# Kernel tuning notes

Hardware: AMD Instinct MI355X
Metric: run time of the kernel (lower is better)

The kernel has to match this reference:

```python
import jax, jax.numpy as jnp
import numpy as np
import math

B, T, D, H = 128, 512, 512, 512


def setup_inputs() -> dict:
    key = jax.random.key(0)
    ks = jax.random.split(key, 6)
    s = 1.0 / math.sqrt(H)
    return {
        "values": jax.random.normal(ks[0], (B, T, D), jnp.float32),
        "Deltas": jax.random.uniform(ks[1], (B, T, D), jnp.float32),
        "W_att": jax.random.normal(ks[2], (D, D), jnp.float32) * s,
        "b_att": jnp.zeros((D,), jnp.float32),
        "W_ih": jax.random.normal(ks[3], (4 * H, D), jnp.float32) * s,
        "W_hh": jax.random.normal(ks[4], (4 * H, H), jnp.float32) * s,
        "b_ih": jnp.zeros((4 * H,), jnp.float32),
        "b_hh": jnp.zeros((4 * H,), jnp.float32),
    }


def lstm_cell(x, h, c, W_ih, W_hh, b_ih, b_hh):
    # torch.nn.LSTMCell: gates ordered i, f, g, o
    g = x @ W_ih.T + b_ih + h @ W_hh.T + b_hh
    i, f, gg, o = jnp.split(g, 4, axis=-1)
    c2 = jax.nn.sigmoid(f) * c + jax.nn.sigmoid(i) * jnp.tanh(gg)
    h2 = jax.nn.sigmoid(o) * jnp.tanh(c2)
    return h2, c2


def reference(values, Deltas, W_att, b_att, W_ih, W_hh, b_ih, b_hh):
    Bn, Tn, Dn = values.shape
    Hn = W_hh.shape[1]
    # cumsum over time then reverse along time (reverse_tensor)
    Del = jnp.flip(jnp.cumsum(Deltas, axis=-2), axis=1)  # [B,T,D]
    v_att = values @ W_att.T + b_att                      # attn-projected inputs [B,T,D]
    # a_ij = bmm(atten_linear(values), values^T) -> [B,T,T]
    a_ij = jnp.einsum('btd,bsd->bts', v_att, values)
    h0 = jnp.zeros((Bn, Hn), values.dtype)
    c0 = jnp.zeros((Bn, Hn), values.dtype)

    def step(carry, x_t):
        h, c = carry
        h2, c2 = lstm_cell(x_t, h, c, W_ih, W_hh, b_ih, b_hh)
        return (h2, c2), (h2, c2)

    xs = jnp.swapaxes(v_att[:, :-1], 0, 1)  # [T-1, B, D]
    (h_last, _), (hs, cs) = jax.lax.scan(step, (h0, c0), xs)
    hs = jnp.swapaxes(hs, 0, 1)  # [B, T-1, H]
    cs = jnp.swapaxes(cs, 0, 1)  # [B, T-1, H]

    # attention-weighted cell-state mixing for the final step
    alpha = jax.nn.softmax(a_ij[:, -1, :-1], axis=-1)[..., None]  # [B,T-1,1]
    d = Del[:, 1:]                                                # [B,T-1,D]
    C_i = jnp.sum(alpha * cs / jnp.log(math.e + d), axis=1)       # [B,H]

    hT, cT = lstm_cell(v_att[:, -1], h_last, C_i, W_ih, W_hh, b_ih, b_hh)
    h_n = jnp.concatenate([hs, hT[:, None, :]], axis=1)  # [B,T,H]
    return h_n
```

## Files before the change

### kernel.cpp

```cpp
#include <hip/hip_runtime.h>
#include <cstdint>

#define DEVI __device__ __forceinline__

typedef unsigned short ushort_t;
typedef __attribute__((ext_vector_type(8))) short s16x8;
typedef __attribute__((ext_vector_type(4))) float f32x4;

DEVI ushort_t f2bf(float f) {
  uint32_t u = __builtin_bit_cast(uint32_t, f);
  u += 0x7fffu + ((u >> 16) & 1u);
  return (ushort_t)(u >> 16);
}
DEVI float bf2f(ushort_t u) {
  uint32_t x = ((uint32_t)u) << 16;
  return __builtin_bit_cast(float, x);
}
DEVI float sigmoidf_(float x) { return 1.0f / (1.0f + __expf(-x)); }
DEVI float tanhf_(float x) {
  float e = __expf(-2.0f * fabsf(x));
  float r = (1.0f - e) / (1.0f + e);
  return copysignf(r, x);
}

DEVI void issue_load_h16(s16x8& dst, const ushort_t* p) {
  asm volatile("global_load_dwordx4 %0, %1, off sc0 sc1" : "=v"(dst) : "v"(p));
}
DEVI int load_flag(const int* p) {
  int r;
  asm volatile("global_load_dword %0, %1, off sc0 sc1\n\ts_waitcnt vmcnt(0)"
               : "=v"(r) : "v"(p) : "memory");
  return r;
}
DEVI void store_h(ushort_t* p, uint32_t v) {
  asm volatile("global_store_short %0, %1, off sc0 sc1" :: "v"(p), "v"(v) : "memory");
}
DEVI void store_flag(int* p, int v) {
  asm volatile("global_store_dword %0, %1, off sc0 sc1" :: "v"(p), "v"(v) : "memory");
}
DEVI void wait_vm0() { asm volatile("s_waitcnt vmcnt(0)" ::: "memory"); }

__global__ void cast_kernel(const float* __restrict__ in, ushort_t* __restrict__ out, long n) {
  long i = ((long)blockIdx.x * blockDim.x + threadIdx.x) * 8;
  if (i >= n) return;
  float4 a = *(const float4*)(in + i);
  float4 b = *(const float4*)(in + i + 4);
  union { s16x8 v; ushort_t u[8]; } r;
  r.u[0] = f2bf(a.x); r.u[1] = f2bf(a.y); r.u[2] = f2bf(a.z); r.u[3] = f2bf(a.w);
  r.u[4] = f2bf(b.x); r.u[5] = f2bf(b.y); r.u[6] = f2bf(b.z); r.u[7] = f2bf(b.w);
  *(s16x8*)(out + i) = r.v;
}

__global__ void transpose512(const float* __restrict__ in, float* __restrict__ out) {
  __shared__ float tile[32][33];
  int bx = blockIdx.x * 32, by = blockIdx.y * 32;
  int tx = threadIdx.x, ty = threadIdx.y;
  for (int i = 0; i < 32; i += 8)
    tile[ty + i][tx] = in[(by + ty + i) * 512 + bx + tx];
  __syncthreads();
  for (int i = 0; i < 32; i += 8)
    out[(bx + ty + i) * 512 + by + tx] = tile[tx][ty + i];
}

__global__ __launch_bounds__(256, 2)
void gemm_bt(const ushort_t* __restrict__ A, const ushort_t* __restrict__ B,
             const float* __restrict__ bias0, const float* __restrict__ bias1,
             ushort_t* __restrict__ C, int N, int K) {
  __shared__ __align__(16) ushort_t As[128 * 64];
  __shared__ __align__(16) ushort_t Bs[128 * 64];
  const int tid = threadIdx.x;
  const int lane = tid & 63, wv = tid >> 6;
  const int wm = wv >> 1, wn = wv & 1;
  const int l15 = lane & 15, l4 = lane >> 4;
  const long m0 = (long)blockIdx.x * 128;
  const int n0 = blockIdx.y * 128;
  const int nkt = K / 64;

  f32x4 acc[4][4] = {};

  int soff[4];
#pragma unroll
  for (int i = 0; i < 4; ++i) {
    int c = tid + i * 256;
    int r = c >> 3, ks = c & 7;
    soff[i] = r * 64 + ((ks ^ (r & 7)) << 3);
  }

#pragma unroll
  for (int i = 0; i < 4; ++i) {
    int c = tid + i * 256; int r = c >> 3; int ks = c & 7;
    *(s16x8*)&As[soff[i]] = *(const s16x8*)&A[(m0 + r) * K + ks * 8];
    *(s16x8*)&Bs[soff[i]] = *(const s16x8*)&B[(long)(n0 + r) * K + ks * 8];
  }
  __syncthreads();

  for (int kt = 0; kt < nkt; ++kt) {
    s16x8 ra[4], rb[4];
    const bool more = (kt + 1 < nkt);
    if (more) {
      const long kb = (long)(kt + 1) * 64;
#pragma unroll
      for (int i = 0; i < 4; ++i) {
        int c = tid + i * 256; int r = c >> 3; int ks = c & 7;
        ra[i] = *(const s16x8*)&A[(m0 + r) * K + kb + ks * 8];
        rb[i] = *(const s16x8*)&B[(long)(n0 + r) * K + kb + ks * 8];
      }
    }
#pragma unroll
    for (int kk = 0; kk < 2; ++kk) {
      s16x8 af[4], bfv[4];
      int slot = kk * 4 + l4;
#pragma unroll
      for (int i = 0; i < 4; ++i) {
        int rA = wm * 64 + i * 16 + l15;
        af[i] = *(const s16x8*)&As[rA * 64 + ((slot ^ (rA & 7)) << 3)];
        int rB = wn * 64 + i * 16 + l15;
        bfv[i] = *(const s16x8*)&Bs[rB * 64 + ((slot ^ (rB & 7)) << 3)];
      }
#pragma unroll
      for (int i = 0; i < 4; ++i)
#pragma unroll
        for (int j = 0; j < 4; ++j)
          acc[i][j] = __builtin_amdgcn_mfma_f32_16x16x32_bf16(af[i], bfv[j], acc[i][j], 0, 0, 0);
    }
    __syncthreads();
    if (more) {
#pragma unroll
      for (int i = 0; i < 4; ++i) {
        *(s16x8*)&As[soff[i]] = ra[i];
        *(s16x8*)&Bs[soff[i]] = rb[i];
      }
      __syncthreads();
    }
  }
#pragma unroll
  for (int i = 0; i < 4; ++i) {
#pragma unroll
    for (int j = 0; j < 4; ++j) {
#pragma unroll
      for (int r = 0; r < 4; ++r) {
        long m = m0 + wm * 64 + i * 16 + l4 * 4 + r;
        int n = n0 + wn * 64 + j * 16 + l15;
        float v = acc[i][j][r] + bias0[n];
        if (bias1) v += bias1[n];
        C[m * (long)N + n] = f2bf(v);
      }
    }
  }
}

__global__ void vT_kernel(const float* __restrict__ values, const float* __restrict__ W_attT,
                          const float* __restrict__ b_att, float* __restrict__ vT) {
  int b = blockIdx.y;
  int n = blockIdx.x * 256 + threadIdx.x;
  __shared__ float xr[512];
  const float* row = values + ((long)b * 512 + 511) * 512;
  for (int k = threadIdx.x; k < 512; k += 256) xr[k] = row[k];
  __syncthreads();
  float acc = b_att[n];
  for (int k = 0; k < 512; ++k) acc += xr[k] * W_attT[k * 512 + n];
  vT[b * 512 + n] = acc;
}

__global__ void dtot_kernel(const float* __restrict__ Deltas, float* __restrict__ Dtot) {
  int idx = blockIdx.x * 256 + threadIdx.x;
  int b = idx >> 9, ch = idx & 511;
  const float* p = Deltas + (long)b * 512 * 512 + ch;
  float s = 0.0f;
  for (int t = 0; t < 511; ++t) s += p[(long)t * 512];
  Dtot[idx] = s;
}

__global__ void logits_kernel(const float* __restrict__ values, const float* __restrict__ vT,
                              float* __restrict__ logits) {
  int b = blockIdx.y;
  int wave = threadIdx.x >> 6, lane = threadIdx.x & 63;
  float vreg[8];
  const float* vtb = vT + b * 512;
#pragma unroll
  for (int j = 0; j < 8; ++j) vreg[j] = vtb[lane * 8 + j];
  int s0 = blockIdx.x * 64 + wave * 16;
  for (int si = 0; si < 16; ++si) {
    int s = s0 + si;
    if (s >= 511) break;
    const float* row = values + ((long)b * 512 + s) * 512 + lane * 8;
    float4 a = *(const float4*)row;
    float4 c = *(const float4*)(row + 4);
    float d = a.x * vreg[0] + a.y * vreg[1] + a.z * vreg[2] + a.w * vreg[3] +
              c.x * vreg[4] + c.y * vreg[5] + c.z * vreg[6] + c.w * vreg[7];
#pragma unroll
    for (int off = 32; off; off >>= 1) d += __shfl_xor(d, off);
    if (lane == 0) logits[b * 512 + s] = d;
  }
}

__global__ void softmax_kernel(float* __restrict__ logits) {
  int b = blockIdx.x, tid = threadIdx.x;
  __shared__ float wmax[4], wsum[4];
  float v0 = (tid < 511) ? logits[b * 512 + tid] : -1e30f;
  float v1 = (tid + 256 < 511) ? logits[b * 512 + tid + 256] : -1e30f;
  float m = fmaxf(v0, v1);
#pragma unroll
  for (int off = 32; off; off >>= 1) m = fmaxf(m, __shfl_xor(m, off));
  if ((tid & 63) == 0) wmax[tid >> 6] = m;
  __syncthreads();
  m = fmaxf(fmaxf(wmax[0], wmax[1]), fmaxf(wmax[2], wmax[3]));
  float e0 = (tid < 511) ? __expf(v0 - m) : 0.0f;
  float e1 = (tid + 256 < 511) ? __expf(v1 - m) : 0.0f;
  float s = e0 + e1;
#pragma unroll
  for (int off = 32; off; off >>= 1) s += __shfl_xor(s, off);
  if ((tid & 63) == 0) wsum[tid >> 6] = s;
  __syncthreads();
  s = wsum[0] + wsum[1] + wsum[2] + wsum[3];
  float inv = 1.0f / s;
  __syncthreads();
  if (tid < 511) logits[b * 512 + tid] = e0 * inv;
  if (tid + 256 < 511) logits[b * 512 + tid + 256] = e1 * inv;
}

__global__ __launch_bounds__(256, 1)
void scan_kernel(const float* __restrict__ W_hh, const ushort_t* __restrict__ Gx,
                 const float* __restrict__ alpha, const float* __restrict__ Dtot,
                 const float* __restrict__ Deltas, ushort_t* __restrict__ hbuf,
                 int* __restrict__ flags, float* __restrict__ out) {
  __shared__ __align__(16) ushort_t whh[64 * 512];
  __shared__ float gbuf[4][16][17];
  const int tid = threadIdx.x;
  const int bg = blockIdx.x & 7, hc = blockIdx.x >> 3;
  const int b0 = bg * 16, n0 = hc * 16;
  const int lane = tid & 63, wv = tid >> 6;
  const int l15 = lane & 15, l4 = lane >> 4;
  const int eb = tid >> 4, eh = tid & 15;
  const int bglob = b0 + eb, hglob = n0 + eh;

  for (int idx = tid; idx < 64 * 512; idx += 256) {
    int r = idx >> 9, k = idx & 511;
    int grow = (r >> 4) * 512 + n0 + (r & 15);
    float v = W_hh[(long)grow * 512 + k];
    int off = r * 512 + ((((k >> 3) ^ (r & 7)) << 3) | (k & 7));
    whh[off] = f2bf(v);
  }
  float c_state = 0.0f, Cacc = 0.0f;
  float running = Dtot[bglob * 512 + hglob];
  __syncthreads();

  const int brow = wv * 16 + l15;
  s16x8 bfr[16];
#pragma unroll
  for (int kk = 0; kk < 16; ++kk) {
    int slot = (kk * 4 + l4) ^ (brow & 7);
    bfr[kk] = *(const s16x8*)&whh[brow * 512 + (slot << 3)];
  }
  const long gxcol = wv * 512 + n0 + l15;

  for (int t = 0; t < 512; ++t) {
    float a_t = 0.0f, delta_t = 0.0f;
    if (t < 511) {
      a_t = alpha[bglob * 512 + t];
      delta_t = Deltas[((long)bglob * 512 + (510 - t)) * 512 + hglob];
    }
    float gx[4];
#pragma unroll
    for (int r = 0; r < 4; ++r)
      gx[r] = bf2f(Gx[((long)(b0 + l4 * 4 + r) * 512 + t) * 2048 + gxcol]);

    if (t > 0) {
      if (wv == 0) {
        const int* fp = flags + ((long)bg * 512 + (t - 1)) * 32 + (lane & 31);
        int g = 0;
        while (!__all(load_flag(fp) != 0)) {
          __builtin_amdgcn_s_sleep(1);
          if (++g > (1 << 20)) break;
        }
      }
      __syncthreads();
    }

    const ushort_t* hb = hbuf + ((t & 1) * 8 + bg) * (16 * 512);
    s16x8 afr[16];
#pragma unroll
    for (int kk = 0; kk < 16; ++kk)
      issue_load_h16(afr[kk], hb + l15 * 512 + kk * 32 + l4 * 8);
    wait_vm0();
    __builtin_amdgcn_sched_barrier(0);

    f32x4 acc = {0.0f, 0.0f, 0.0f, 0.0f};
#pragma unroll
    for (int kk = 0; kk < 16; ++kk)
      acc = __builtin_amdgcn_mfma_f32_16x16x32_bf16(afr[kk], bfr[kk], acc, 0, 0, 0);
#pragma unroll
    for (int r = 0; r < 4; ++r)
      gbuf[wv][l4 * 4 + r][l15] = acc[r] + gx[r];
    __syncthreads();

    float gi = gbuf[0][eb][eh], gf = gbuf[1][eb][eh];
    float gg = gbuf[2][eb][eh], go = gbuf[3][eb][eh];
    float cin = (t == 511) ? Cacc : c_state;
    float cnew = sigmoidf_(gf) * cin + sigmoidf_(gi) * tanhf_(gg);
    float hnew = sigmoidf_(go) * tanhf_(cnew);
    out[((long)bglob * 512 + t) * 512 + hglob] = hnew;
    if (t < 511) {
      c_state = cnew;
      float rl = 1.0f / __logf(2.71828182845904523f + running);
      Cacc += a_t * cnew * rl;
      running -= delta_t;
      ushort_t* hw = hbuf + (((t + 1) & 1) * 8 + bg) * (16 * 512);
      store_h(hw + eb * 512 + hglob, (uint32_t)f2bf(hnew));
      wait_vm0();
      __syncthreads();
      if (tid == 0)
        store_flag(flags + ((long)bg * 512 + t) * 32 + hc, 1);
    }
  }
}

extern "C" void kernel_launch(void* const* d_in, const int* in_sizes, int n_in,
                              void* d_out, int out_size, void* d_ws, size_t ws_size,
                              hipStream_t stream) {
  const float* values = (const float*)d_in[0];
  const float* Deltas = (const float*)d_in[1];
  const float* W_att  = (const float*)d_in[2];
  const float* b_att  = (const float*)d_in[3];
  const float* W_ih   = (const float*)d_in[4];
  const float* W_hh   = (const float*)d_in[5];
  const float* b_ih   = (const float*)d_in[6];
  const float* b_hh   = (const float*)d_in[7];
  float* out = (float*)d_out;

  char* ws = (char*)d_ws;
  size_t off = 0;
  auto alloc = [&](size_t bytes) -> void* {
    void* p = ws + off;
    off += (bytes + 255) & ~(size_t)255;
    return p;
  };
  ushort_t* values_bf = (ushort_t*)alloc(67108864ull);
  ushort_t* v_att_bf  = (ushort_t*)alloc(67108864ull);
  ushort_t* Gx        = (ushort_t*)alloc(268435456ull);
  ushort_t* W_att_bf  = (ushort_t*)alloc(524288ull);
  ushort_t* W_ih_bf   = (ushort_t*)alloc(2097152ull);
  float*    W_attT    = (float*)alloc(1048576ull);
  float*    vT        = (float*)alloc(262144ull);
  float*    Dtot      = (float*)alloc(262144ull);
  float*    alpha     = (float*)alloc(262144ull);
  ushort_t* hbuf      = (ushort_t*)alloc(262144ull);
  int*      flags     = (int*)alloc(524288ull);

  hipMemsetAsync(hbuf, 0, 262144ull + 524288ull, stream);

  cast_kernel<<<33554432 / 8 / 256, 256, 0, stream>>>(values, values_bf, 33554432L);
  cast_kernel<<<262144 / 8 / 256, 256, 0, stream>>>(W_att, W_att_bf, 262144L);
  cast_kernel<<<1048576 / 8 / 256, 256, 0, stream>>>(W_ih, W_ih_bf, 1048576L);
  transpose512<<<dim3(16, 16), dim3(32, 8), 0, stream>>>(W_att, W_attT);

  gemm_bt<<<dim3(512, 4), 256, 0, stream>>>(values_bf, W_att_bf, b_att, nullptr,
                                            v_att_bf, 512, 512);
  gemm_bt<<<dim3(512, 16), 256, 0, stream>>>(v_att_bf, W_ih_bf, b_ih, b_hh,
                                             Gx, 2048, 512);

  vT_kernel<<<dim3(2, 128), 256, 0, stream>>>(values, W_attT, b_att, vT);
  dtot_kernel<<<256, 256, 0, stream>>>(Deltas, Dtot);
  logits_kernel<<<dim3(8, 128), 256, 0, stream>>>(values, vT, alpha);
  softmax_kernel<<<128, 256, 0, stream>>>(alpha);

  scan_kernel<<<256, 256, 0, stream>>>(W_hh, Gx, alpha, Dtot, Deltas, hbuf, flags, out);
}
```

Before: 2.528 ms.

## Fold W_att into W_ih and replace flag barrier with tagged h values

Precomputes the combined weight W_ih·W_att and its bias, so the input-gate GEMM reads values directly and the separate v_att projection GEMM is removed. The scan kernel drops the per-step flag array and block barrier: each h element is stored as a 32-bit word holding the step tag and the bf16 value, and readers spin until every tag matches. The MFMA work is reorganised so each wave covers a K-slice for all four gates, with the partial sums reduced through double-buffered shared memory. This cuts GEMM traffic and per-step synchronisation latency, at the cost of doubling the h buffer size and rounding the fused weight to bf16.

```diff
diff --git a/kernel.cpp b/kernel.cpp
--- a/kernel.cpp
+++ b/kernel.cpp
@@ -5,6 +5,7 @@
 
 typedef unsigned short ushort_t;
 typedef __attribute__((ext_vector_type(8))) short s16x8;
+typedef __attribute__((ext_vector_type(4))) int i32x4;
 typedef __attribute__((ext_vector_type(4))) float f32x4;
 
 DEVI ushort_t f2bf(float f) {
@@ -23,19 +24,10 @@
   return copysignf(r, x);
 }
 
-DEVI void issue_load_h16(s16x8& dst, const ushort_t* p) {
+DEVI void load_tag16(i32x4& dst, const uint32_t* p) {
   asm volatile("global_load_dwordx4 %0, %1, off sc0 sc1" : "=v"(dst) : "v"(p));
 }
-DEVI int load_flag(const int* p) {
-  int r;
-  asm volatile("global_load_dword %0, %1, off sc0 sc1\n\ts_waitcnt vmcnt(0)"
-               : "=v"(r) : "v"(p) : "memory");
-  return r;
-}
-DEVI void store_h(ushort_t* p, uint32_t v) {
-  asm volatile("global_store_short %0, %1, off sc0 sc1" :: "v"(p), "v"(v) : "memory");
-}
-DEVI void store_flag(int* p, int v) {
+DEVI void store_tagged(uint32_t* p, uint32_t v) {
   asm volatile("global_store_dword %0, %1, off sc0 sc1" :: "v"(p), "v"(v) : "memory");
 }
 DEVI void wait_vm0() { asm volatile("s_waitcnt vmcnt(0)" ::: "memory"); }
@@ -141,12 +133,26 @@
       for (int r = 0; r < 4; ++r) {
         long m = m0 + wm * 64 + i * 16 + l4 * 4 + r;
         int n = n0 + wn * 64 + j * 16 + l15;
-        float v = acc[i][j][r] + bias0[n];
+        float v = acc[i][j][r];
+        if (bias0) v += bias0[n];
         if (bias1) v += bias1[n];
         C[m * (long)N + n] = f2bf(v);
       }
     }
   }
+}
+
+__global__ void bias_combo_kernel(const float* __restrict__ W_ih, const float* __restrict__ b_att,
+                                  const float* __restrict__ b_ih, const float* __restrict__ b_hh,
+                                  float* __restrict__ bc) {
+  int n = blockIdx.x * 256 + threadIdx.x;
+  __shared__ float ba[512];
+  for (int k = threadIdx.x; k < 512; k += 256) ba[k] = b_att[k];
+  __syncthreads();
+  float s = b_ih[n] + b_hh[n];
+  const float* row = W_ih + (long)n * 512;
+  for (int k = 0; k < 512; ++k) s += row[k] * ba[k];
+  bc[n] = s;
 }
 
 __global__ void vT_kernel(const float* __restrict__ values, const float* __restrict__ W_attT,
@@ -222,10 +228,10 @@
 __global__ __launch_bounds__(256, 1)
 void scan_kernel(const float* __restrict__ W_hh, const ushort_t* __restrict__ Gx,
                  const float* __restrict__ alpha, const float* __restrict__ Dtot,
-                 const float* __restrict__ Deltas, ushort_t* __restrict__ hbuf,
-                 int* __restrict__ flags, float* __restrict__ out) {
+                 const float* __restrict__ Deltas, uint32_t* __restrict__ hbuf32,
+                 float* __restrict__ out) {
   __shared__ __align__(16) ushort_t whh[64 * 512];
-  __shared__ float gbuf[4][16][17];
+  __shared__ float gbuf[2][4][4][16][16];
   const int tid = threadIdx.x;
   const int bg = blockIdx.x & 7, hc = blockIdx.x >> 3;
   const int b0 = bg * 16, n0 = hc * 16;
@@ -245,14 +251,17 @@
   float running = Dtot[bglob * 512 + hglob];
   __syncthreads();
 
-  const int brow = wv * 16 + l15;
-  s16x8 bfr[16];
-#pragma unroll
-  for (int kk = 0; kk < 16; ++kk) {
-    int slot = (kk * 4 + l4) ^ (brow & 7);
-    bfr[kk] = *(const s16x8*)&whh[brow * 512 + (slot << 3)];
-  }
-  const long gxcol = wv * 512 + n0 + l15;
+  s16x8 bfr[4][4];
+#pragma unroll
+  for (int g = 0; g < 4; ++g) {
+    const int brow = g * 16 + l15;
+#pragma unroll
+    for (int kk4 = 0; kk4 < 4; ++kk4) {
+      int ks = wv * 128 + kk4 * 32 + l4 * 8;
+      int slot = (ks >> 3) ^ (brow & 7);
+      bfr[g][kk4] = *(const s16x8*)&whh[brow * 512 + (slot << 3)];
+    }
+  }
 
   for (int t = 0; t < 512; ++t) {
     float a_t = 0.0f, delta_t = 0.0f;
@@ -260,57 +269,76 @@
       a_t = alpha[bglob * 512 + t];
       delta_t = Deltas[((long)bglob * 512 + (510 - t)) * 512 + hglob];
     }
-    float gx[4];
-#pragma unroll
-    for (int r = 0; r < 4; ++r)
-      gx[r] = bf2f(Gx[((long)(b0 + l4 * 4 + r) * 512 + t) * 2048 + gxcol]);
-
-    if (t > 0) {
-      if (wv == 0) {
-        const int* fp = flags + ((long)bg * 512 + (t - 1)) * 32 + (lane & 31);
-        int g = 0;
-        while (!__all(load_flag(fp) != 0)) {
-          __builtin_amdgcn_s_sleep(1);
-          if (++g > (1 << 20)) break;
-        }
-      }
-      __syncthreads();
-    }
-
-    const ushort_t* hb = hbuf + ((t & 1) * 8 + bg) * (16 * 512);
-    s16x8 afr[16];
-#pragma unroll
-    for (int kk = 0; kk < 16; ++kk)
-      issue_load_h16(afr[kk], hb + l15 * 512 + kk * 32 + l4 * 8);
-    wait_vm0();
-    __builtin_amdgcn_sched_barrier(0);
-
-    f32x4 acc = {0.0f, 0.0f, 0.0f, 0.0f};
-#pragma unroll
-    for (int kk = 0; kk < 16; ++kk)
-      acc = __builtin_amdgcn_mfma_f32_16x16x32_bf16(afr[kk], bfr[kk], acc, 0, 0, 0);
-#pragma unroll
-    for (int r = 0; r < 4; ++r)
-      gbuf[wv][l4 * 4 + r][l15] = acc[r] + gx[r];
+    float gxv[4];
+#pragma unroll
+    for (int g = 0; g < 4; ++g)
+      gxv[g] = bf2f(Gx[((long)bglob * 512 + t) * 2048 + g * 512 + hglob]);
+
+    const uint32_t* hb = hbuf32 + ((t & 1) * 8 + bg) * 8192 + l15 * 512 + wv * 128 + l4 * 8;
+    const uint32_t expect = (uint32_t)t << 16;
+    i32x4 q[8];
+    int guard = 0;
+    for (;;) {
+#pragma unroll
+      for (int kk4 = 0; kk4 < 4; ++kk4) {
+        load_tag16(q[kk4 * 2], hb + kk4 * 32);
+        load_tag16(q[kk4 * 2 + 1], hb + kk4 * 32 + 4);
+      }
+      wait_vm0();
+      __builtin_amdgcn_sched_barrier(0);
+      uint32_t bad = 0;
+#pragma unroll
+      for (int i = 0; i < 8; ++i) {
+        bad |= (uint32_t)q[i][0] ^ expect;
+        bad |= (uint32_t)q[i][1] ^ expect;
+        bad |= (uint32_t)q[i][2] ^ expect;
+        bad |= (uint32_t)q[i][3] ^ expect;
+      }
+      if (!__any((bad & 0xffff0000u) != 0)) break;
+      __builtin_amdgcn_s_sleep(1);
+      if (++guard > (1 << 16)) break;
+    }
+    s16x8 afr[4];
+#pragma unroll
+    for (int kk4 = 0; kk4 < 4; ++kk4) {
+#pragma unroll
+      for (int j = 0; j < 4; ++j) {
+        afr[kk4][j]     = (short)((uint32_t)q[kk4 * 2][j] & 0xffffu);
+        afr[kk4][j + 4] = (short)((uint32_t)q[kk4 * 2 + 1][j] & 0xffffu);
+      }
+    }
+    f32x4 acc[4] = {};
+#pragma unroll
+    for (int kk4 = 0; kk4 < 4; ++kk4)
+#pragma unroll
+      for (int g = 0; g < 4; ++g)
+        acc[g] = __builtin_amdgcn_mfma_f32_16x16x32_bf16(afr[kk4], bfr[g][kk4], acc[g], 0, 0, 0);
+
+    const int p = t & 1;
+#pragma unroll
+    for (int g = 0; g < 4; ++g)
+#pragma unroll
+      for (int r = 0; r < 4; ++r)
+        gbuf[p][wv][g][l4 * 4 + r][l15] = acc[g][r];
     __syncthreads();
 
-    float gi = gbuf[0][eb][eh], gf = gbuf[1][eb][eh];
-    float gg = gbuf[2][eb][eh], go = gbuf[3][eb][eh];
+    float gate[4];
+#pragma unroll
+    for (int g = 0; g < 4; ++g)
+      gate[g] = gbuf[p][0][g][eb][eh] + gbuf[p][1][g][eb][eh] +
+                gbuf[p][2][g][eb][eh] + gbuf[p][3][g][eb][eh] + gxv[g];
+
     float cin = (t == 511) ? Cacc : c_state;
-    float cnew = sigmoidf_(gf) * cin + sigmoidf_(gi) * tanhf_(gg);
-    float hnew = sigmoidf_(go) * tanhf_(cnew);
+    float cnew = sigmoidf_(gate[1]) * cin + sigmoidf_(gate[0]) * tanhf_(gate[2]);
+    float hnew = sigmoidf_(gate[3]) * tanhf_(cnew);
     out[((long)bglob * 512 + t) * 512 + hglob] = hnew;
     if (t < 511) {
       c_state = cnew;
       float rl = 1.0f / __logf(2.71828182845904523f + running);
       Cacc += a_t * cnew * rl;
       running -= delta_t;
-      ushort_t* hw = hbuf + (((t + 1) & 1) * 8 + bg) * (16 * 512);
-      store_h(hw + eb * 512 + hglob, (uint32_t)f2bf(hnew));
-      wait_vm0();
-      __syncthreads();
-      if (tid == 0)
-        store_flag(flags + ((long)bg * 512 + t) * 32 + hc, 1);
+      uint32_t w = ((uint32_t)(t + 1) << 16) | (uint32_t)f2bf(hnew);
+      store_tagged(hbuf32 + (((t + 1) & 1) * 8 + bg) * 8192 + eb * 512 + hglob, w);
     }
   }
 }
@@ -336,27 +364,29 @@
     return p;
   };
   ushort_t* values_bf = (ushort_t*)alloc(67108864ull);
-  ushort_t* v_att_bf  = (ushort_t*)alloc(67108864ull);
   ushort_t* Gx        = (ushort_t*)alloc(268435456ull);
-  ushort_t* W_att_bf  = (ushort_t*)alloc(524288ull);
   ushort_t* W_ih_bf   = (ushort_t*)alloc(2097152ull);
+  ushort_t* Wc_bf     = (ushort_t*)alloc(2097152ull);
   float*    W_attT    = (float*)alloc(1048576ull);
+  ushort_t* W_attT_bf = (ushort_t*)alloc(524288ull);
   float*    vT        = (float*)alloc(262144ull);
   float*    Dtot      = (float*)alloc(262144ull);
   float*    alpha     = (float*)alloc(262144ull);
-  ushort_t* hbuf      = (ushort_t*)alloc(262144ull);
-  int*      flags     = (int*)alloc(524288ull);
-
-  hipMemsetAsync(hbuf, 0, 262144ull + 524288ull, stream);
+  float*    bias_c    = (float*)alloc(8192ull);
+  uint32_t* hbuf32    = (uint32_t*)alloc(524288ull);
+
+  hipMemsetAsync(hbuf32, 0, 524288ull, stream);
 
   cast_kernel<<<33554432 / 8 / 256, 256, 0, stream>>>(values, values_bf, 33554432L);
-  cast_kernel<<<262144 / 8 / 256, 256, 0, stream>>>(W_att, W_att_bf, 262144L);
   cast_kernel<<<1048576 / 8 / 256, 256, 0, stream>>>(W_ih, W_ih_bf, 1048576L);
   transpose512<<<dim3(16, 16), dim3(32, 8), 0, stream>>>(W_att, W_attT);
-
-  gemm_bt<<<dim3(512, 4), 256, 0, stream>>>(values_bf, W_att_bf, b_att, nullptr,
-                                            v_att_bf, 512, 512);
-  gemm_bt<<<dim3(512, 16), 256, 0, stream>>>(v_att_bf, W_ih_bf, b_ih, b_hh,
+  cast_kernel<<<262144 / 8 / 256, 256, 0, stream>>>(W_attT, W_attT_bf, 262144L);
+
+  gemm_bt<<<dim3(16, 4), 256, 0, stream>>>(W_ih_bf, W_attT_bf, nullptr, nullptr,
+                                           Wc_bf, 512, 512);
+  bias_combo_kernel<<<8, 256, 0, stream>>>(W_ih, b_att, b_ih, b_hh, bias_c);
+
+  gemm_bt<<<dim3(512, 16), 256, 0, stream>>>(values_bf, Wc_bf, bias_c, nullptr,
                                              Gx, 2048, 512);
 
   vT_kernel<<<dim3(2, 128), 256, 0, stream>>>(values, W_attT, b_att, vT);
@@ -364,5 +394,5 @@
   logits_kernel<<<dim3(8, 128), 256, 0, stream>>>(values, vT, alpha);
   softmax_kernel<<<128, 256, 0, stream>>>(alpha);
 
-  scan_kernel<<<256, 256, 0, stream>>>(W_hh, Gx, alpha, Dtot, Deltas, hbuf, flags, out);
-}
+  scan_kernel<<<256, 256, 0, stream>>>(W_hh, Gx, alpha, Dtot, Deltas, hbuf32, out);
+}
```

Result: faster. 2.285 ms (-9.6%).
